# Kernel tuning notes

Hardware: AMD Instinct MI355X
Metric: run time of the kernel (lower is better)

Reference implementation:

```python
import jax, jax.numpy as jnp
import numpy as np
from jax import lax

B, N, H, W, C = 8, 1024, 256, 256, 256
HID = 512
RATES = (1, 3, 9, 9, 3, 1)


def setup_inputs() -> dict:
    key = jax.random.key(0)
    ks = jax.random.split(key, 16)
    # vertices are (row, col) float coordinates inside the feature map
    vertices = jax.random.uniform(ks[0], (B, N, 2), jnp.float32) * jnp.array([H - 1, W - 1], jnp.float32)
    features = jax.random.normal(ks[1], (B, H, W, C), jnp.float32)
    inp = {"vertices": vertices, "features": features}
    # Conv1D stack params (haiku Conv1D: kernel [K, Cin, Cout], bias [Cout])
    cin = C
    for i in range(6):
        inp[f"w{i}"] = jax.random.normal(ks[2 + 2 * i], (3, cin, HID), jnp.float32) * 0.05
        inp[f"b{i}"] = jax.random.normal(ks[3 + 2 * i], (HID,), jnp.float32) * 0.05
        cin = HID
    # offset head: Conv1D(2, 1, with_bias=False); original zero-init, randomized here
    inp["w_off"] = jax.random.normal(ks[14], (1, HID, 2), jnp.float32) * 0.05
    return inp


def _conv1d(x, w, b, rate):
    # x: [B, N, Cin], w: [K, Cin, Cout] -> SAME-padded dilated conv over vertex axis
    y = lax.conv_general_dilated(x, w, window_strides=(1,), padding="SAME",
                                 rhs_dilation=(rate,),
                                 dimension_numbers=("NWC", "WIO", "NWC"))
    return y if b is None else y + b


def _sample_at_vertices(vertices, features):
    # bilinear interpolation, zero outside (map_coordinates order=1 mode='constant')
    Bb, Hh, Ww, Cc = features.shape
    y, x = vertices[..., 0], vertices[..., 1]  # [B, N]
    y0f, x0f = jnp.floor(y), jnp.floor(x)
    wy1, wx1 = y - y0f, x - x0f
    wy0, wx0 = 1.0 - wy1, 1.0 - wx1
    y0, x0 = y0f.astype(jnp.int32), x0f.astype(jnp.int32)
    flat = features.reshape(Bb, Hh * Ww, Cc)

    def gather(yi, xi, wgt):
        valid = (yi >= 0) & (yi < Hh) & (xi >= 0) & (xi < Ww)
        idx = jnp.clip(yi, 0, Hh - 1) * Ww + jnp.clip(xi, 0, Ww - 1)  # [B, N]
        vals = jnp.take_along_axis(flat, idx[..., None], axis=1)  # [B, N, C]
        return vals * (wgt * valid)[..., None]

    return (gather(y0, x0, wy0 * wx0) + gather(y0, x0 + 1, wy0 * wx1)
            + gather(y0 + 1, x0, wy1 * wx0) + gather(y0 + 1, x0 + 1, wy1 * wx1))


def reference(vertices, features, w0, b0, w1, b1, w2, b2, w3, b3, w4, b4, w5, b5, w_off):
    h = _sample_at_vertices(vertices, features)  # [B, N, C]
    ws = (w0, w1, w2, w3, w4, w5)
    bs = (b0, b1, b2, b3, b4, b5)
    for w, b, r in zip(ws, bs, RATES):
        h = jax.nn.relu(_conv1d(h, w, b, r))
    offsets = _conv1d(h, w_off, None, 1)  # [B, N, 2]
    return vertices + offsets
```

## Files before the change

### kernel.cpp

```cpp
#include <hip/hip_runtime.h>

#define BATCH 8
#define NPTS  1024
#define FH    256
#define FW    256
#define FC    256
#define HID   512
#define PADN  1056
#define HALO  16

typedef __attribute__((ext_vector_type(8))) short short8;
typedef __attribute__((ext_vector_type(16))) float f32x16;
typedef unsigned short ushort_t;
typedef unsigned int uint_t;

__device__ __forceinline__ ushort_t f2bf(float f) {
    uint_t u = __builtin_bit_cast(uint_t, f);
    u += 0x7fffu + ((u >> 16) & 1u);
    return (ushort_t)(u >> 16);
}
__device__ __forceinline__ float bf2f(ushort_t s) {
    uint_t u = ((uint_t)s) << 16;
    return __builtin_bit_cast(float, u);
}

#define GLOAD16(g, l)                                                     \
    __builtin_amdgcn_global_load_lds(                                     \
        (const __attribute__((address_space(1))) void*)(g),               \
        (__attribute__((address_space(3))) void*)(l), 16, 0, 0)

__global__ __launch_bounds__(256) void prep_kernel(
    const float* __restrict__ vertices, const float* __restrict__ features,
    const float* __restrict__ w0, const float* __restrict__ w1,
    const float* __restrict__ w2, const float* __restrict__ w3,
    const float* __restrict__ w4, const float* __restrict__ w5,
    ushort_t* __restrict__ wt0, ushort_t* __restrict__ wt1,
    ushort_t* __restrict__ wt2, ushort_t* __restrict__ wt3,
    ushort_t* __restrict__ wt4, ushort_t* __restrict__ wt5,
    ushort_t* __restrict__ XpA, ushort_t* __restrict__ XpB,
    ushort_t* __restrict__ XpC)
{
    __shared__ float tile[64][65];
    const int blk = blockIdx.x;
    const int tid = threadIdx.x;

    if (blk < 1280) {
        int i = blk * 256 + tid;
        if (i < 65536) {
            int b = i >> 13, rem = i & 8191;
            int strip = rem >> 12, off = rem & 4095;
            XpA[(size_t)b * (PADN * FC) + (strip ? (PADN - HALO) * FC : 0) + off] = 0;
        }
        int jB = i - 65536;
        if (jB >= 0 && jB < 262144) {
            ushort_t* T = (jB < 131072) ? XpB : XpC;
            int j = jB & 131071;
            int b = j >> 14, rem = j & 16383;
            int strip = rem >> 13, off = rem & 8191;
            T[(size_t)b * (PADN * HID) + (strip ? (PADN - HALO) * HID : 0) + off] = 0;
        }
        return;
    }

    if (blk < 2336) {
        int j = blk - 1280;
        const float* w; ushort_t* wt; int CIN, kk0, co0;
        if (j < 96) {
            w = w0; wt = wt0; CIN = FC;
            kk0 = (j % 12) * 64; co0 = (j / 12) * 64;
        } else {
            int j2 = j - 96;
            int layer = j2 / 192, jj = j2 % 192;
            const float* ws[5]  = {w1, w2, w3, w4, w5};
            ushort_t*   wts[5]  = {wt1, wt2, wt3, wt4, wt5};
            w = ws[layer]; wt = wts[layer]; CIN = HID;
            kk0 = (jj % 24) * 64; co0 = (jj / 24) * 64;
        }
        int tap = kk0 / CIN, ci0 = kk0 - tap * CIN;
        int K3 = 3 * CIN;
#pragma unroll 4
        for (int it = 0; it < 16; ++it) {
            int r = it * 4 + (tid >> 6);
            tile[r][tid & 63] = w[((size_t)tap * CIN + ci0 + r) * HID + co0 + (tid & 63)];
        }
        __syncthreads();
#pragma unroll 4
        for (int it = 0; it < 16; ++it) {
            int co = it * 4 + (tid >> 6);
            wt[(size_t)(co0 + co) * K3 + kk0 + (tid & 63)] = f2bf(tile[tid & 63][co]);
        }
        return;
    }

    {
        int p = (blk - 2336) * 4 + (tid >> 6);
        int b = p >> 10;
        int n = p & 1023;
        int t = tid & 63;

        float y = vertices[2 * p + 0];
        float x = vertices[2 * p + 1];
        float y0f = floorf(y), x0f = floorf(x);
        float wy1 = y - y0f, wx1 = x - x0f;
        float wy0 = 1.f - wy1, wx0 = 1.f - wx1;
        int y0 = (int)y0f, x0 = (int)x0f;

        float4 acc = make_float4(0.f, 0.f, 0.f, 0.f);
        const float4* fbase = (const float4*)features + (size_t)b * FH * FW * (FC / 4);

#define CORNER(yi, xi, wgt) {                                                  \
        int yy = (yi), xx = (xi);                                              \
        float wv = ((yy >= 0) && (yy < FH) && (xx >= 0) && (xx < FW)) ? (wgt) : 0.f; \
        int yc = yy < 0 ? 0 : (yy > FH - 1 ? FH - 1 : yy);                     \
        int xc = xx < 0 ? 0 : (xx > FW - 1 ? FW - 1 : xx);                     \
        float4 v = fbase[((size_t)yc * FW + xc) * (FC / 4) + t];               \
        acc.x += v.x * wv; acc.y += v.y * wv; acc.z += v.z * wv; acc.w += v.w * wv; }

        CORNER(y0,     x0,     wy0 * wx0);
        CORNER(y0,     x0 + 1, wy0 * wx1);
        CORNER(y0 + 1, x0,     wy1 * wx0);
        CORNER(y0 + 1, x0 + 1, wy1 * wx1);
#undef CORNER

        ushort4 o;
        o.x = f2bf(acc.x); o.y = f2bf(acc.y); o.z = f2bf(acc.z); o.w = f2bf(acc.w);
        *(ushort4*)(XpA + ((size_t)b * PADN + HALO + n) * FC + 4 * t) = o;
    }
}

template <int CIN>
__global__ __launch_bounds__(256) void conv_mfma(
    const ushort_t* __restrict__ Xp,
    const ushort_t* __restrict__ Wt,
    const float* __restrict__ bias,
    ushort_t* __restrict__ Yp,
    int rate)
{
    constexpr int K3 = 3 * CIN;
    constexpr int NT = K3 / 64;
    __shared__ short lds[2][12288];

    const int tid  = threadIdx.x;
    const int wid  = tid >> 6;
    const int lane = tid & 63;
    const int wm   = wid >> 1, wn = wid & 1;

    const int h  = blockIdx.x;
    const int bm = (h & 7) * 8 + (h >> 6);
    const int bn = (h >> 3) & 7;
    const int batch = bm >> 3;
    const int n0    = (bm & 7) * 128;
    const int co0   = bn * 64;

    const short* Xbase = (const short*)Xp + ((size_t)batch * PADN + HALO + n0) * CIN;
    const short* Wbase = (const short*)Wt + (size_t)co0 * K3;

    auto stage = [&](int buf, int kt) {
        const int tap = (kt << 6) / CIN;
        const int ci0 = (kt << 6) - tap * CIN;
        const short* Ag = Xbase + (ptrdiff_t)(tap - 1) * rate * CIN + ci0;
        const short* Bg = Wbase + (kt << 6);
        short* ldsA = &lds[buf][0];
        short* ldsB = &lds[buf][8192];
#pragma unroll
        for (int it = 0; it < 4; ++it) {
            int row  = wid * 32 + it * 8 + (lane >> 3);
            int chnk = (lane & 7) ^ (row & 7);
            GLOAD16(Ag + (size_t)row * CIN + chnk * 8, ldsA + ((wid * 4 + it) << 9));
        }
#pragma unroll
        for (int it = 0; it < 2; ++it) {
            int row  = wid * 16 + it * 8 + (lane >> 3);
            int chnk = (lane & 7) ^ (row & 7);
            GLOAD16(Bg + (size_t)row * K3 + chnk * 8, ldsB + ((wid * 2 + it) << 9));
        }
    };

    f32x16 acc[2];
    const int rowA0 = wm * 64 + (lane & 31);
    const int coB   = wn * 32 + (lane & 31);
    {
        float bv = bias[co0 + coB];
#pragma unroll
        for (int i = 0; i < 2; ++i)
#pragma unroll
            for (int r = 0; r < 16; ++r) acc[i][r] = bv;
    }

    stage(0, 0);
    asm volatile("s_waitcnt vmcnt(0)" ::: "memory");
    __syncthreads();

    int cur = 0;
    for (int kt = 0; kt < NT; ++kt) {
        if (kt + 1 < NT) stage(cur ^ 1, kt + 1);

        const short* As = &lds[cur][0];
        const short* Bs = &lds[cur][8192];
#pragma unroll
        for (int ks = 0; ks < 4; ++ks) {
            int ch = ks * 2 + (lane >> 5);
            short8 av[2], bv;
#pragma unroll
            for (int i = 0; i < 2; ++i) {
                int ra = rowA0 + i * 32;
                av[i] = *(const short8*)(As + ra * 64 + ((ch ^ (ra & 7)) << 3));
            }
            bv = *(const short8*)(Bs + coB * 64 + ((ch ^ (coB & 7)) << 3));
#pragma unroll
            for (int i = 0; i < 2; ++i)
                acc[i] = __builtin_amdgcn_mfma_f32_32x32x16_bf16(
                    av[i], bv, acc[i], 0, 0, 0);
        }
        __syncthreads();
        cur ^= 1;
    }

    ushort_t* Yb = Yp + ((size_t)batch * PADN + HALO + n0) * HID + co0;
#pragma unroll
    for (int i = 0; i < 2; ++i) {
#pragma unroll
        for (int r = 0; r < 16; ++r) {
            int rrow = wm * 64 + i * 32 + (r & 3) + 8 * (r >> 2) + 4 * (lane >> 5);
            float v = acc[i][r];
            v = v > 0.f ? v : 0.f;
            Yb[(size_t)rrow * HID + coB] = f2bf(v);
        }
    }
}

__global__ __launch_bounds__(64) void head_kernel(
    const ushort_t* __restrict__ h, const float* __restrict__ w_off,
    const float* __restrict__ vertices, float* __restrict__ out)
{
    int p = blockIdx.x;
    int b = p >> 10, n = p & 1023;
    int t = threadIdx.x;
    const ushort_t* hr = h + ((size_t)b * PADN + HALO + n) * HID + t * 8;

    uint4 raw = *(const uint4*)hr;
    ushort_t hv[8];
    hv[0] = raw.x & 0xffff; hv[1] = raw.x >> 16;
    hv[2] = raw.y & 0xffff; hv[3] = raw.y >> 16;
    hv[4] = raw.z & 0xffff; hv[5] = raw.z >> 16;
    hv[6] = raw.w & 0xffff; hv[7] = raw.w >> 16;

    float s0 = 0.f, s1 = 0.f;
#pragma unroll
    for (int k = 0; k < 8; ++k) {
        float x = bf2f(hv[k]);
        s0 += x * w_off[(t * 8 + k) * 2 + 0];
        s1 += x * w_off[(t * 8 + k) * 2 + 1];
    }
#pragma unroll
    for (int off = 32; off >= 1; off >>= 1) {
        s0 += __shfl_down(s0, off);
        s1 += __shfl_down(s1, off);
    }
    if (t == 0) {
        out[2 * p + 0] = vertices[2 * p + 0] + s0;
        out[2 * p + 1] = vertices[2 * p + 1] + s1;
    }
}

extern "C" void kernel_launch(void* const* d_in, const int* in_sizes, int n_in,
                              void* d_out, int out_size, void* d_ws, size_t ws_size,
                              hipStream_t stream)
{
    (void)in_sizes; (void)n_in; (void)out_size; (void)ws_size;

    const float* vertices = (const float*)d_in[0];
    const float* features = (const float*)d_in[1];
    const float* w[6]  = {(const float*)d_in[2], (const float*)d_in[4],
                          (const float*)d_in[6], (const float*)d_in[8],
                          (const float*)d_in[10], (const float*)d_in[12]};
    const float* bb[6] = {(const float*)d_in[3], (const float*)d_in[5],
                          (const float*)d_in[7], (const float*)d_in[9],
                          (const float*)d_in[11], (const float*)d_in[13]};
    const float* w_off = (const float*)d_in[14];
    float* out = (float*)d_out;

    char* p = (char*)d_ws;
    ushort_t* wt[6];
    wt[0] = (ushort_t*)p; p += (size_t)HID * (3 * FC) * 2;
    for (int i = 1; i < 6; ++i) { wt[i] = (ushort_t*)p; p += (size_t)HID * (3 * HID) * 2; }
    ushort_t* XpA = (ushort_t*)p; p += (size_t)BATCH * PADN * FC  * 2;
    ushort_t* XpB = (ushort_t*)p; p += (size_t)BATCH * PADN * HID * 2;
    ushort_t* XpC = (ushort_t*)p;

    prep_kernel<<<4384, 256, 0, stream>>>(
        vertices, features, w[0], w[1], w[2], w[3], w[4], w[5],
        wt[0], wt[1], wt[2], wt[3], wt[4], wt[5], XpA, XpB, XpC);

    static const int rates[6] = {1, 3, 9, 9, 3, 1};
    conv_mfma<FC><<<512, 256, 0, stream>>>(XpA, wt[0], bb[0], XpB, rates[0]);
    ushort_t* src = XpB;
    ushort_t* dst = XpC;
    for (int i = 1; i < 6; ++i) {
        conv_mfma<HID><<<512, 256, 0, stream>>>(src, wt[i], bb[i], dst, rates[i]);
        ushort_t* tmp = src; src = dst; dst = tmp;
    }

    head_kernel<<<BATCH * NPTS, 64, 0, stream>>>(src, w_off, vertices, out);
}
```

Measured before the change: 126.1 us.

## Widen conv GEMM tile to 128x128 with 2x2 MFMA per wave and lighter sync

The conv GEMM block tile grows from 128x64 to 128x128 output channels, so each wave computes a 2x2 grid of 32x32 MFMA tiles and reuses each A fragment twice. The grid halves from 512 to 256 blocks. The pipeline now waits with a partial vmcnt so the next stage's loads can stay in flight, uses raw s_barrier with sched_barrier, and raises wave priority during the MFMA section. This cuts LDS and global traffic per FLOP, but 256 blocks is roughly one block per CU, so occupancy and latency hiding may suffer.

```diff
diff --git a/kernel.cpp b/kernel.cpp
--- a/kernel.cpp
+++ b/kernel.cpp
@@ -138,19 +138,20 @@
 {
     constexpr int K3 = 3 * CIN;
     constexpr int NT = K3 / 64;
-    __shared__ short lds[2][12288];
+    __shared__ short lds[2][16384];
 
     const int tid  = threadIdx.x;
     const int wid  = tid >> 6;
     const int lane = tid & 63;
     const int wm   = wid >> 1, wn = wid & 1;
 
-    const int h  = blockIdx.x;
-    const int bm = (h & 7) * 8 + (h >> 6);
-    const int bn = (h >> 3) & 7;
+    const int h   = blockIdx.x;
+    const int loc = h >> 3;
+    const int bm  = (h & 7) * 8 + (loc >> 2);
+    const int bn  = loc & 3;
     const int batch = bm >> 3;
     const int n0    = (bm & 7) * 128;
-    const int co0   = bn * 64;
+    const int co0   = bn * 128;
 
     const short* Xbase = (const short*)Xp + ((size_t)batch * PADN + HALO + n0) * CIN;
     const short* Wbase = (const short*)Wt + (size_t)co0 * K3;
@@ -167,66 +168,79 @@
             int row  = wid * 32 + it * 8 + (lane >> 3);
             int chnk = (lane & 7) ^ (row & 7);
             GLOAD16(Ag + (size_t)row * CIN + chnk * 8, ldsA + ((wid * 4 + it) << 9));
-        }
-#pragma unroll
-        for (int it = 0; it < 2; ++it) {
-            int row  = wid * 16 + it * 8 + (lane >> 3);
-            int chnk = (lane & 7) ^ (row & 7);
-            GLOAD16(Bg + (size_t)row * K3 + chnk * 8, ldsB + ((wid * 2 + it) << 9));
+            GLOAD16(Bg + (size_t)row * K3  + chnk * 8, ldsB + ((wid * 4 + it) << 9));
         }
     };
 
-    f32x16 acc[2];
+    f32x16 acc[2][2];
     const int rowA0 = wm * 64 + (lane & 31);
-    const int coB   = wn * 32 + (lane & 31);
-    {
-        float bv = bias[co0 + coB];
+    const int rowB0 = wn * 64 + (lane & 31);
+#pragma unroll
+    for (int j = 0; j < 2; ++j) {
+        float bv = bias[co0 + wn * 64 + j * 32 + (lane & 31)];
 #pragma unroll
         for (int i = 0; i < 2; ++i)
 #pragma unroll
-            for (int r = 0; r < 16; ++r) acc[i][r] = bv;
+            for (int r = 0; r < 16; ++r) acc[i][j][r] = bv;
     }
 
     stage(0, 0);
-    asm volatile("s_waitcnt vmcnt(0)" ::: "memory");
-    __syncthreads();
 
     int cur = 0;
     for (int kt = 0; kt < NT; ++kt) {
-        if (kt + 1 < NT) stage(cur ^ 1, kt + 1);
+        if (kt + 1 < NT) {
+            stage(cur ^ 1, kt + 1);
+            asm volatile("s_waitcnt vmcnt(8)" ::: "memory");
+        } else {
+            asm volatile("s_waitcnt vmcnt(0)" ::: "memory");
+        }
+        __builtin_amdgcn_s_barrier();
+        __builtin_amdgcn_sched_barrier(0);
 
         const short* As = &lds[cur][0];
         const short* Bs = &lds[cur][8192];
+        __builtin_amdgcn_s_setprio(1);
 #pragma unroll
         for (int ks = 0; ks < 4; ++ks) {
             int ch = ks * 2 + (lane >> 5);
-            short8 av[2], bv;
+            short8 av[2], bv[2];
 #pragma unroll
             for (int i = 0; i < 2; ++i) {
                 int ra = rowA0 + i * 32;
                 av[i] = *(const short8*)(As + ra * 64 + ((ch ^ (ra & 7)) << 3));
             }
-            bv = *(const short8*)(Bs + coB * 64 + ((ch ^ (coB & 7)) << 3));
+#pragma unroll
+            for (int j = 0; j < 2; ++j) {
+                int rb = rowB0 + j * 32;
+                bv[j] = *(const short8*)(Bs + rb * 64 + ((ch ^ (rb & 7)) << 3));
+            }
 #pragma unroll
             for (int i = 0; i < 2; ++i)
-                acc[i] = __builtin_amdgcn_mfma_f32_32x32x16_bf16(
-                    av[i], bv, acc[i], 0, 0, 0);
-        }
-        __syncthreads();
+#pragma unroll
+                for (int j = 0; j < 2; ++j)
+                    acc[i][j] = __builtin_amdgcn_mfma_f32_32x32x16_bf16(
+                        av[i], bv[j], acc[i][j], 0, 0, 0);
+        }
+        __builtin_amdgcn_s_setprio(0);
+        __builtin_amdgcn_sched_barrier(0);
+        __builtin_amdgcn_s_barrier();
         cur ^= 1;
     }
 
     ushort_t* Yb = Yp + ((size_t)batch * PADN + HALO + n0) * HID + co0;
 #pragma unroll
-    for (int i = 0; i < 2; ++i) {
-#pragma unroll
-        for (int r = 0; r < 16; ++r) {
-            int rrow = wm * 64 + i * 32 + (r & 3) + 8 * (r >> 2) + 4 * (lane >> 5);
-            float v = acc[i][r];
-            v = v > 0.f ? v : 0.f;
-            Yb[(size_t)rrow * HID + coB] = f2bf(v);
-        }
-    }
+    for (int i = 0; i < 2; ++i)
+#pragma unroll
+        for (int j = 0; j < 2; ++j) {
+            int cco = wn * 64 + j * 32 + (lane & 31);
+#pragma unroll
+            for (int r = 0; r < 16; ++r) {
+                int rrow = wm * 64 + i * 32 + (r & 3) + 8 * (r >> 2) + 4 * (lane >> 5);
+                float v = acc[i][j][r];
+                v = v > 0.f ? v : 0.f;
+                Yb[(size_t)rrow * HID + cco] = f2bf(v);
+            }
+        }
 }
 
 __global__ __launch_bounds__(64) void head_kernel(
@@ -293,11 +307,11 @@
         wt[0], wt[1], wt[2], wt[3], wt[4], wt[5], XpA, XpB, XpC);
 
     static const int rates[6] = {1, 3, 9, 9, 3, 1};
-    conv_mfma<FC><<<512, 256, 0, stream>>>(XpA, wt[0], bb[0], XpB, rates[0]);
+    conv_mfma<FC><<<256, 256, 0, stream>>>(XpA, wt[0], bb[0], XpB, rates[0]);
     ushort_t* src = XpB;
     ushort_t* dst = XpC;
     for (int i = 1; i < 6; ++i) {
-        conv_mfma<HID><<<512, 256, 0, stream>>>(src, wt[i], bb[i], dst, rates[i]);
+        conv_mfma<HID><<<256, 256, 0, stream>>>(src, wt[i], bb[i], dst, rates[i]);
         ushort_t* tmp = src; src = dst; dst = tmp;
     }
 
```

Result: slower. 132.3 us (+4.9%).
